# Performance work log

Hardware: AMD Instinct MI355X
Metric: run time of the kernel (lower is better)

The kernel has to match this reference:

```python
import jax, jax.numpy as jnp
import numpy as np

NEG_SLOPE = 0.2
EPS = 1e-16  # PyG softmax denominator epsilon


def add_self_loops(edge_index, num_nodes):
    loop = jnp.arange(num_nodes, dtype=edge_index.dtype)
    src = jnp.concatenate([edge_index[0], loop])
    dst = jnp.concatenate([edge_index[1], loop])
    return src, dst


def gat_conv(x, src, dst, W, att_src, att_dst, bias, num_nodes):
    H, C = att_src.shape
    h = (x @ W).reshape(num_nodes, H, C)            # [N,H,C]
    a_s = jnp.einsum('nhc,hc->nh', h, att_src)      # [N,H]
    a_d = jnp.einsum('nhc,hc->nh', h, att_dst)
    e = jax.nn.leaky_relu(a_s[src] + a_d[dst], NEG_SLOPE)  # [E,H]
    m = jax.ops.segment_max(e, dst, num_segments=num_nodes)
    e = jnp.exp(e - m[dst])
    s = jax.ops.segment_sum(e, dst, num_segments=num_nodes)
    alpha = e / (s[dst] + EPS)                      # [E,H]
    out = jax.ops.segment_sum(h[src] * alpha[:, :, None], dst,
                              num_segments=num_nodes)  # [N,H,C]
    return out.reshape(num_nodes, H * C) + bias


def setup_inputs() -> dict:
    key = jax.random.key(0)
    ks = jax.random.split(key, 10)
    N, E, F, Ch = 50000, 800000, 128, 64
    sc = lambda f: 1.0 / np.sqrt(f)
    return {
        'x': jax.random.normal(ks[0], (N, F), jnp.float32),
        'edge_index': jax.random.randint(ks[1], (2, E), 0, N, jnp.int64),
        'W1': jax.random.normal(ks[2], (F, 4 * Ch), jnp.float32) * sc(F),
        'att_src1': jax.random.normal(ks[3], (4, Ch), jnp.float32) * sc(Ch),
        'att_dst1': jax.random.normal(ks[4], (4, Ch), jnp.float32) * sc(Ch),
        'b1': jnp.zeros((4 * Ch,), jnp.float32),
        'W2': jax.random.normal(ks[5], (4 * Ch, Ch), jnp.float32) * sc(4 * Ch),
        'att_src2': jax.random.normal(ks[6], (1, Ch), jnp.float32) * sc(Ch),
        'att_dst2': jax.random.normal(ks[7], (1, Ch), jnp.float32) * sc(Ch),
        'b2': jnp.zeros((Ch,), jnp.float32),
    }


def reference(x, edge_index, W1, att_src1, att_dst1, b1, W2, att_src2, att_dst2, b2):
    N = x.shape[0]
    src, dst = add_self_loops(edge_index, N)
    # dropout layers are inference no-ops
    h = gat_conv(x, src, dst, W1, att_src1, att_dst1, b1, N)
    h = jax.nn.elu(h)
    out = gat_conv(h, src, dst, W2, att_src2, att_dst2, b2, N)
    return out
```

## Files before the change

kernel.cpp:

```cpp
#include <hip/hip_runtime.h>
#include <hip/hip_bf16.h>
#include <stdint.h>


typedef __attribute__((ext_vector_type(8))) short bf16x8;
typedef __attribute__((ext_vector_type(4))) float f32x4;

__device__ __forceinline__ float bf2f(__hip_bfloat16 v) { return __bfloat162float(v); }
__device__ __forceinline__ float bfbits2f(unsigned short s) {
  union { uint32_t u; float f; } v; v.u = ((uint32_t)s) << 16; return v.f;
}
__device__ __forceinline__ unsigned short f2bfbits(float f) {
  union { float f; uint32_t u; } v; v.f = f;
  uint32_t u = v.u;
  return (unsigned short)((u + 0x7fffu + ((u >> 16) & 1u)) >> 16);
}

template <bool BF>
__device__ __forceinline__ float loadF(const void* p, size_t i) {
  if (BF) return bf2f(((const __hip_bfloat16*)p)[i]);
  return ((const float*)p)[i];
}
template <bool BF>
__device__ __forceinline__ void storeF(void* p, size_t i, float v) {
  if (BF) ((__hip_bfloat16*)p)[i] = __float2bfloat16(v);
  else    ((float*)p)[i] = v;
}
template <bool I64>
__device__ __forceinline__ int loadI(const void* p, size_t i) {
  if (I64) return (int)((const long long*)p)[i];
  return ((const int*)p)[i];
}
__device__ __forceinline__ float lrelu(float v) { return fmaxf(v, 0.2f * v); }

__global__ void detect_kernel(const uint32_t* __restrict__ xbits,
                              const uint32_t* __restrict__ eibits,
                              int* __restrict__ flags) {
  if (threadIdx.x != 0 || blockIdx.x != 0) return;
  int plausible = 0;
  for (int i = 0; i < 64; i++) {
    uint32_t u = xbits[i];
    uint32_t e = (u >> 23) & 0xffu;
    if ((e < 160u && e > 90u) || (u & 0x7fffffffu) == 0u) plausible++;
  }
  flags[0] = (plausible < 32) ? 1 : 0;
  int allz = 1;
  for (int i = 0; i < 64; i++)
    if (eibits[2 * i + 1] != 0u) allz = 0;
  flags[1] = allz;
}

__global__ __launch_bounds__(256) void prep_all(
    const void* __restrict__ x, unsigned short* __restrict__ xb, size_t nx,
    const void* __restrict__ W1, unsigned short* __restrict__ w1t, int K1, int N1,
    const void* __restrict__ W2, unsigned short* __restrict__ w2t, int K2, int N2,
    int nb_cast, int nb_t1, const int* __restrict__ flags) {
  const int b = blockIdx.x;
  const bool f = flags[0] != 0;
  if (b < nb_cast) {
    size_t i = ((size_t)b * 256 + threadIdx.x) * 4;
    if (i >= nx) return;
    ushort4 o;
    if (f) {
      o = *(const ushort4*)((const unsigned short*)x + i);
    } else {
      float4 v = *(const float4*)((const float*)x + i);
      o.x = f2bfbits(v.x); o.y = f2bfbits(v.y);
      o.z = f2bfbits(v.z); o.w = f2bfbits(v.w);
    }
    *(ushort4*)(xb + i) = o;
  } else if (b < nb_cast + nb_t1) {
    int idx = (b - nb_cast) * 256 + threadIdx.x;
    if (idx >= K1 * N1) return;
    int k = idx / N1, n = idx - k * N1;
    float v = f ? loadF<true>(W1, idx) : loadF<false>(W1, idx);
    w1t[(size_t)n * K1 + k] = f2bfbits(v);
  } else {
    int idx = (b - nb_cast - nb_t1) * 256 + threadIdx.x;
    if (idx >= K2 * N2) return;
    int k = idx / N2, n = idx - k * N2;
    float v = f ? loadF<true>(W2, idx) : loadF<false>(W2, idx);
    w2t[(size_t)n * K2 + k] = f2bfbits(v);
  }
}

template <int KC, int NT, int HB>
__global__ __launch_bounds__(256, 4) void gemm_mfma_att(
    const unsigned short* __restrict__ A,
    const unsigned short* __restrict__ BT,
    unsigned short* __restrict__ C,
    const void* __restrict__ att_s, const void* __restrict__ att_d,
    float* __restrict__ as_o, float* __restrict__ ad_o,
    float* __restrict__ wself_o,
    int M, int Htot, const int* __restrict__ flags) {
  const int lane = threadIdx.x & 63;
  const int col = lane & 15;
  const int quad = lane >> 4;
  const int m0 = blockIdx.x * 64 + (threadIdx.x >> 6) * 16;
  const int n0 = blockIdx.y * (NT * 16);
  const int NCOL = Htot * 64;

  int gm = m0 + col;
  if (gm > M - 1) gm = M - 1;
  const unsigned short* arow = A + (size_t)gm * KC + quad * 8;
  const unsigned short* bbase = BT + (size_t)(n0 + col) * KC + quad * 8;

  f32x4 acc[NT] = {};
#pragma unroll
  for (int k0 = 0; k0 < KC; k0 += 32) {
    bf16x8 a = *(const bf16x8*)(arow + k0);
#pragma unroll
    for (int s = 0; s < NT; s++) {
      bf16x8 b = *(const bf16x8*)(bbase + (size_t)s * 16 * KC + k0);
      acc[s] = __builtin_amdgcn_mfma_f32_16x16x32_bf16(a, b, acc[s], 0, 0, 0);
    }
  }
#pragma unroll
  for (int s = 0; s < NT; s++)
#pragma unroll
    for (int r = 0; r < 4; r++) {
      int m = m0 + quad * 4 + r;
      if (m < M) C[(size_t)m * NCOL + n0 + s * 16 + col] = f2bfbits(acc[s][r]);
    }
  const int SC = NT / HB;
  const bool f = flags[0] != 0;
#pragma unroll
  for (int h = 0; h < HB; h++) {
    const int gh = blockIdx.y * HB + h;
    float ps[4] = {0.f, 0.f, 0.f, 0.f};
    float pd[4] = {0.f, 0.f, 0.f, 0.f};
#pragma unroll
    for (int j = 0; j < SC; j++) {
      int s = h * SC + j;
      int ci = gh * 64 + j * 16 + col;
      float av = f ? loadF<true>(att_s, ci) : loadF<false>(att_s, ci);
      float dv = f ? loadF<true>(att_d, ci) : loadF<false>(att_d, ci);
#pragma unroll
      for (int r = 0; r < 4; r++) {
        ps[r] += acc[s][r] * av;
        pd[r] += acc[s][r] * dv;
      }
    }
#pragma unroll
    for (int o = 1; o < 16; o <<= 1) {
#pragma unroll
      for (int r = 0; r < 4; r++) {
        ps[r] += __shfl_xor(ps[r], o);
        pd[r] += __shfl_xor(pd[r], o);
      }
    }
    if (col == 0) {
#pragma unroll
      for (int r = 0; r < 4; r++) {
        int m = m0 + quad * 4 + r;
        if (m < M) {
          as_o[m * Htot + gh] = ps[r];
          ad_o[m * Htot + gh] = pd[r];
          wself_o[m * Htot + gh] = __expf(lrelu(ps[r] + pd[r]));
        }
      }
    }
  }
}

__global__ void hist_kernel(const void* __restrict__ ei, int E,
                            int* __restrict__ deg, const int* __restrict__ flags) {
  int e = blockIdx.x * blockDim.x + threadIdx.x;
  if (e >= E) return;
  int d = flags[1] ? loadI<true>(ei, (size_t)E + e) : loadI<false>(ei, (size_t)E + e);
  atomicAdd(&deg[d], 1);
}

__global__ __launch_bounds__(256) void scan_block_sums(const int* __restrict__ deg,
                                                       int* __restrict__ bsum, int n) {
  __shared__ int buf[256];
  const int t = threadIdx.x;
  const int i = blockIdx.x * 256 + t;
  buf[t] = (i < n) ? deg[i] : 0;
  __syncthreads();
  for (int o = 128; o > 0; o >>= 1) {
    if (t < o) buf[t] += buf[t + o];
    __syncthreads();
  }
  if (t == 0) bsum[blockIdx.x] = buf[0];
}

__global__ __launch_bounds__(256) void scan_bsums(int* __restrict__ bsum, int nb) {
  __shared__ int buf[256];
  const int t = threadIdx.x;
  int orig = (t < nb) ? bsum[t] : 0;
  buf[t] = orig;
  __syncthreads();
  for (int o = 1; o < 256; o <<= 1) {
    int v = (t >= o) ? buf[t - o] : 0;
    __syncthreads();
    buf[t] += v;
    __syncthreads();
  }
  if (t < nb) bsum[t] = buf[t] - orig;
}

__global__ __launch_bounds__(256) void scan_finalize(const int* __restrict__ deg,
                                                     const int* __restrict__ bsum,
                                                     int* __restrict__ row_start, int n) {
  __shared__ int buf[256];
  const int t = threadIdx.x;
  const int i = blockIdx.x * 256 + t;
  int v = (i < n) ? deg[i] : 0;
  buf[t] = v;
  __syncthreads();
  for (int o = 1; o < 256; o <<= 1) {
    int x = (t >= o) ? buf[t - o] : 0;
    __syncthreads();
    buf[t] += x;
    __syncthreads();
  }
  if (i < n) row_start[i + 1] = bsum[blockIdx.x] + buf[t];
  if (i == 0) row_start[0] = 0;
}

__global__ void scatter_edges(const void* __restrict__ ei, int E,
                              const int* __restrict__ row_start,
                              int* __restrict__ cursor, int* __restrict__ col_src,
                              int* __restrict__ col_dst,
                              const int* __restrict__ flags) {
  int e = blockIdx.x * blockDim.x + threadIdx.x;
  if (e >= E) return;
  int s, d;
  if (flags[1]) { s = loadI<true>(ei, e);  d = loadI<true>(ei, (size_t)E + e); }
  else          { s = loadI<false>(ei, e); d = loadI<false>(ei, (size_t)E + e); }
  int pos = atomicAdd(&cursor[d], 1);
  int idx = row_start[d] + pos;
  col_src[idx] = s;
  col_dst[idx] = d;
}

__global__ __launch_bounds__(256) void weight4(
    const int* __restrict__ col_src, const int* __restrict__ col_dst,
    const float4* __restrict__ as4, const float4* __restrict__ ad4,
    float4* __restrict__ wbuf, int E) {
  int e = blockIdx.x * 256 + threadIdx.x;
  if (e >= E) return;
  float4 a = as4[col_src[e]];
  float4 b = ad4[col_dst[e]];
  float4 w;
  w.x = __expf(lrelu(a.x + b.x));
  w.y = __expf(lrelu(a.y + b.y));
  w.z = __expf(lrelu(a.z + b.z));
  w.w = __expf(lrelu(a.w + b.w));
  wbuf[e] = w;
}

__global__ __launch_bounds__(256) void weight1(
    const int* __restrict__ col_src, const int* __restrict__ col_dst,
    const float* __restrict__ as_, const float* __restrict__ ad_,
    float* __restrict__ wbuf, int E) {
  int e = blockIdx.x * 256 + threadIdx.x;
  if (e >= E) return;
  wbuf[e] = __expf(lrelu(as_[col_src[e]] + ad_[col_dst[e]]));
}

__global__ __launch_bounds__(256) void aggregate4(
    const unsigned short* __restrict__ h_in,
    const float* __restrict__ wselfA,
    const float* __restrict__ wbuf,
    const int* __restrict__ row_start, const int* __restrict__ col_src,
    const void* __restrict__ bias,
    unsigned short* __restrict__ out,
    int N, const int* __restrict__ flags) {
  const int dst = blockIdx.x * 4 + (threadIdx.x >> 6);
  if (dst >= N) return;
  const int l = threadIdx.x & 63;
  const int h = l >> 4;
  const int rs = row_start[dst];
  const int dg = row_start[dst + 1] - rs;
  const float ws = wselfA[dst * 4 + h];

  float a0, a1, a2, a3;
  {
    ushort4 sv = *(const ushort4*)(h_in + (size_t)dst * 256 + 4 * l);
    a0 = ws * bfbits2f(sv.x);
    a1 = ws * bfbits2f(sv.y);
    a2 = ws * bfbits2f(sv.z);
    a3 = ws * bfbits2f(sv.w);
  }
  float p = 0.f;
#pragma unroll 4
  for (int i = 0; i < dg; i++) {
    int sn = col_src[rs + i];
    float w = wbuf[(size_t)(rs + i) * 4 + h];
    p += w;
    ushort4 sv = *(const ushort4*)(h_in + (size_t)sn * 256 + 4 * l);
    a0 += w * bfbits2f(sv.x);
    a1 += w * bfbits2f(sv.y);
    a2 += w * bfbits2f(sv.z);
    a3 += w * bfbits2f(sv.w);
  }
  const float inv = 1.0f / (p + ws + 1e-16f);
  const bool f = flags[0] != 0;
  float b0, b1, b2, b3;
  if (f) {
    b0 = loadF<true>(bias, 4 * l + 0); b1 = loadF<true>(bias, 4 * l + 1);
    b2 = loadF<true>(bias, 4 * l + 2); b3 = loadF<true>(bias, 4 * l + 3);
  } else {
    b0 = loadF<false>(bias, 4 * l + 0); b1 = loadF<false>(bias, 4 * l + 1);
    b2 = loadF<false>(bias, 4 * l + 2); b3 = loadF<false>(bias, 4 * l + 3);
  }
  float o0 = a0 * inv + b0, o1 = a1 * inv + b1;
  float o2 = a2 * inv + b2, o3 = a3 * inv + b3;
  o0 = o0 > 0.f ? o0 : __expf(o0) - 1.f;
  o1 = o1 > 0.f ? o1 : __expf(o1) - 1.f;
  o2 = o2 > 0.f ? o2 : __expf(o2) - 1.f;
  o3 = o3 > 0.f ? o3 : __expf(o3) - 1.f;
  ushort4 ov;
  ov.x = f2bfbits(o0); ov.y = f2bfbits(o1); ov.z = f2bfbits(o2); ov.w = f2bfbits(o3);
  *(ushort4*)(out + (size_t)dst * 256 + 4 * l) = ov;
}

__global__ __launch_bounds__(256) void aggregate1(
    const unsigned short* __restrict__ h_in,
    const float* __restrict__ wselfA,
    const float* __restrict__ wbuf,
    const int* __restrict__ row_start, const int* __restrict__ col_src,
    const void* __restrict__ bias,
    void* __restrict__ out, int N, const int* __restrict__ flags) {
  const int dst = blockIdx.x * 4 + (threadIdx.x >> 6);
  if (dst >= N) return;
  const int l = threadIdx.x & 63;
  const int el = l & 15;
  const int slot = l >> 4;
  const int rs = row_start[dst];
  const int dg = row_start[dst + 1] - rs;
  const float ws = wselfA[dst];

  float a0 = 0.f, a1 = 0.f, a2 = 0.f, a3 = 0.f, p = 0.f;
  if (slot == 0) {
    ushort4 sv = *(const ushort4*)(h_in + (size_t)dst * 64 + 4 * el);
    a0 = ws * bfbits2f(sv.x);
    a1 = ws * bfbits2f(sv.y);
    a2 = ws * bfbits2f(sv.z);
    a3 = ws * bfbits2f(sv.w);
  }
#pragma unroll 2
  for (int i = slot; i < dg; i += 4) {
    int sn = col_src[rs + i];
    float w = wbuf[rs + i];
    p += w;
    ushort4 sv = *(const ushort4*)(h_in + (size_t)sn * 64 + 4 * el);
    a0 += w * bfbits2f(sv.x);
    a1 += w * bfbits2f(sv.y);
    a2 += w * bfbits2f(sv.z);
    a3 += w * bfbits2f(sv.w);
  }
  a0 += __shfl_xor(a0, 16); a0 += __shfl_xor(a0, 32);
  a1 += __shfl_xor(a1, 16); a1 += __shfl_xor(a1, 32);
  a2 += __shfl_xor(a2, 16); a2 += __shfl_xor(a2, 32);
  a3 += __shfl_xor(a3, 16); a3 += __shfl_xor(a3, 32);
  p  += __shfl_xor(p, 16);  p  += __shfl_xor(p, 32);

  if (slot == 0) {
    const float inv = 1.0f / (p + ws + 1e-16f);
    const bool f = flags[0] != 0;
    float b0, b1, b2, b3;
    if (f) {
      b0 = loadF<true>(bias, 4 * el + 0); b1 = loadF<true>(bias, 4 * el + 1);
      b2 = loadF<true>(bias, 4 * el + 2); b3 = loadF<true>(bias, 4 * el + 3);
    } else {
      b0 = loadF<false>(bias, 4 * el + 0); b1 = loadF<false>(bias, 4 * el + 1);
      b2 = loadF<false>(bias, 4 * el + 2); b3 = loadF<false>(bias, 4 * el + 3);
    }
    float o0 = a0 * inv + b0, o1 = a1 * inv + b1;
    float o2 = a2 * inv + b2, o3 = a3 * inv + b3;
    size_t ob = (size_t)dst * 64 + 4 * el;
    if (f) {
      ushort4 ov;
      ov.x = f2bfbits(o0); ov.y = f2bfbits(o1);
      ov.z = f2bfbits(o2); ov.w = f2bfbits(o3);
      *(ushort4*)((unsigned short*)out + ob) = ov;
    } else {
      float4 ov; ov.x = o0; ov.y = o1; ov.z = o2; ov.w = o3;
      *(float4*)((float*)out + ob) = ov;
    }
  }
}

extern "C" void kernel_launch(void* const* d_in, const int* in_sizes, int n_in,
                              void* d_out, int out_size, void* d_ws, size_t ws_size,
                              hipStream_t stream) {
  const void* x    = d_in[0];
  const void* ei   = d_in[1];
  const void* W1   = d_in[2];
  const void* as1w = d_in[3];
  const void* ad1w = d_in[4];
  const void* b1   = d_in[5];
  const void* W2   = d_in[6];
  const void* as2w = d_in[7];
  const void* ad2w = d_in[8];
  const void* b2   = d_in[9];

  const int N  = out_size / 64;
  const int F  = in_sizes[0] / N;
  const int E  = in_sizes[1] / 2;
  const int H1 = in_sizes[3] / 64;
  const int D1 = H1 * 64;
  const int D2 = 64;

  size_t off = 0;
  auto alloc = [&](size_t bytes) -> void* {
    void* p = (char*)d_ws + off;
    off += (bytes + 255) & ~(size_t)255;
    return p;
  };
  int* flags = (int*)alloc(2 * sizeof(int));
  __hip_bfloat16* h1 = (__hip_bfloat16*)alloc((size_t)N * D1 * 2);
  __hip_bfloat16* x2 = (__hip_bfloat16*)alloc((size_t)N * D1 * 2);
  __hip_bfloat16* h2 = h1;
  unsigned short* xb  = (unsigned short*)alloc((size_t)N * F * 2);
  unsigned short* w1t = (unsigned short*)alloc((size_t)D1 * F * 2);
  unsigned short* w2t = (unsigned short*)alloc((size_t)D2 * D1 * 2);
  float* as1 = (float*)alloc((size_t)N * H1 * 4);
  float* ad1 = (float*)alloc((size_t)N * H1 * 4);
  float* wself1 = (float*)alloc((size_t)N * H1 * 4);
  float* as2 = (float*)alloc((size_t)N * 4);
  float* ad2 = (float*)alloc((size_t)N * 4);
  float* wself2 = (float*)alloc((size_t)N * 4);
  int* zero_region = (int*)alloc((size_t)2 * N * 4);
  int* deg = zero_region;
  int* cursor = zero_region + N;
  int* row_start = (int*)alloc((size_t)(N + 1) * 4);
  int* col_src = (int*)alloc((size_t)E * 4);
  int* col_dst = (int*)alloc((size_t)E * 4);
  float* wbuf = (float*)alloc((size_t)E * 4 * 4);
  int* bsum = (int*)alloc((size_t)256 * 4);
  (void)ws_size; (void)n_in;

  const int nb = (N + 255) / 256;
  const int eb = (E + 255) / 256;
  const int db = (N + 3) / 4;
  const int gb = (N + 63) / 64;

  detect_kernel<<<1, 64, 0, stream>>>((const uint32_t*)x, (const uint32_t*)ei, flags);
  hipMemsetAsync(zero_region, 0, (size_t)2 * N * 4, stream);
  hist_kernel<<<eb, 256, 0, stream>>>(ei, E, deg, flags);
  scan_block_sums<<<nb, 256, 0, stream>>>(deg, bsum, N);
  scan_bsums<<<1, 256, 0, stream>>>(bsum, nb);
  scan_finalize<<<nb, 256, 0, stream>>>(deg, bsum, row_start, N);
  scatter_edges<<<eb, 256, 0, stream>>>(ei, E, row_start, cursor, col_src, col_dst, flags);

  const size_t nx = (size_t)N * F;
  const int nb_cast = (int)((nx / 4 + 255) / 256);
  const int nb_t1 = (F * D1 + 255) / 256;
  const int nb_t2 = (D1 * D2 + 255) / 256;
  prep_all<<<nb_cast + nb_t1 + nb_t2, 256, 0, stream>>>(
      x, xb, nx, W1, w1t, F, D1, W2, w2t, D1, D2, nb_cast, nb_t1, flags);

  gemm_mfma_att<128, 8, 2><<<dim3(gb, 2), 256, 0, stream>>>(
      xb, w1t, (unsigned short*)h1, as1w, ad1w, as1, ad1, wself1, N, H1, flags);
  weight4<<<eb, 256, 0, stream>>>(col_src, col_dst, (const float4*)as1,
                                  (const float4*)ad1, (float4*)wbuf, E);
  aggregate4<<<db, 256, 0, stream>>>((const unsigned short*)h1, wself1, wbuf,
                                     row_start, col_src, b1,
                                     (unsigned short*)x2, N, flags);

  gemm_mfma_att<256, 4, 1><<<dim3(gb, 1), 256, 0, stream>>>(
      (const unsigned short*)x2, w2t, (unsigned short*)h2, as2w, ad2w,
      as2, ad2, wself2, N, 1, flags);
  weight1<<<eb, 256, 0, stream>>>(col_src, col_dst, as2, ad2, wbuf, E);
  aggregate1<<<db, 256, 0, stream>>>((const unsigned short*)h2, wself2, wbuf,
                                     row_start, col_src, b2, d_out, N, flags);
}
```

Measured before the change: 349.4 us.

## Fuse edge attention weight computation into aggregation kernels and merge detect with zeroing

Removes the separate weight4/weight1 kernels and the per-edge wbuf and col_dst buffers. Each aggregation kernel now recomputes exp(leaky_relu(a_s[src]+a_d[dst])) inline from the gathered source index, so an E×4 float buffer no longer has to be written and read back. The format-detection kernel is parallelised with ballots and also zeroes the degree/cursor region, replacing a memset launch. In exchange the aggregate loops do extra scattered loads of a_s per edge and redundant exp work across the lanes of each head.

```diff
diff --git a/kernel.cpp b/kernel.cpp
--- a/kernel.cpp
+++ b/kernel.cpp
@@ -21,11 +21,6 @@
   if (BF) return bf2f(((const __hip_bfloat16*)p)[i]);
   return ((const float*)p)[i];
 }
-template <bool BF>
-__device__ __forceinline__ void storeF(void* p, size_t i, float v) {
-  if (BF) ((__hip_bfloat16*)p)[i] = __float2bfloat16(v);
-  else    ((float*)p)[i] = v;
-}
 template <bool I64>
 __device__ __forceinline__ int loadI(const void* p, size_t i) {
   if (I64) return (int)((const long long*)p)[i];
@@ -33,21 +28,27 @@
 }
 __device__ __forceinline__ float lrelu(float v) { return fmaxf(v, 0.2f * v); }
 
-__global__ void detect_kernel(const uint32_t* __restrict__ xbits,
-                              const uint32_t* __restrict__ eibits,
-                              int* __restrict__ flags) {
-  if (threadIdx.x != 0 || blockIdx.x != 0) return;
-  int plausible = 0;
-  for (int i = 0; i < 64; i++) {
-    uint32_t u = xbits[i];
-    uint32_t e = (u >> 23) & 0xffu;
-    if ((e < 160u && e > 90u) || (u & 0x7fffffffu) == 0u) plausible++;
-  }
-  flags[0] = (plausible < 32) ? 1 : 0;
-  int allz = 1;
-  for (int i = 0; i < 64; i++)
-    if (eibits[2 * i + 1] != 0u) allz = 0;
-  flags[1] = allz;
+__global__ __launch_bounds__(256) void detect_zero(
+    const uint32_t* __restrict__ xbits, const uint32_t* __restrict__ eibits,
+    int* __restrict__ flags, int* __restrict__ zero_region, int nzero) {
+  if (blockIdx.x == 0) {
+    if (threadIdx.x < 64) {
+      const int l = threadIdx.x;
+      uint32_t u = xbits[l];
+      uint32_t e = (u >> 23) & 0xffu;
+      bool plausible = (e < 160u && e > 90u) || (u & 0x7fffffffu) == 0u;
+      unsigned long long m1 = __ballot(plausible);
+      bool z = (eibits[2 * l + 1] == 0u);
+      unsigned long long m2 = __ballot(z);
+      if (l == 0) {
+        flags[0] = (__popcll(m1) < 32) ? 1 : 0;
+        flags[1] = (m2 == ~0ULL) ? 1 : 0;
+      }
+    }
+    return;
+  }
+  int i = (blockIdx.x - 1) * 256 + threadIdx.x;
+  if (i < nzero) zero_region[i] = 0;
 }
 
 __global__ __launch_bounds__(256) void prep_all(
@@ -222,7 +223,6 @@
 __global__ void scatter_edges(const void* __restrict__ ei, int E,
                               const int* __restrict__ row_start,
                               int* __restrict__ cursor, int* __restrict__ col_src,
-                              int* __restrict__ col_dst,
                               const int* __restrict__ flags) {
   int e = blockIdx.x * blockDim.x + threadIdx.x;
   if (e >= E) return;
@@ -230,40 +230,14 @@
   if (flags[1]) { s = loadI<true>(ei, e);  d = loadI<true>(ei, (size_t)E + e); }
   else          { s = loadI<false>(ei, e); d = loadI<false>(ei, (size_t)E + e); }
   int pos = atomicAdd(&cursor[d], 1);
-  int idx = row_start[d] + pos;
-  col_src[idx] = s;
-  col_dst[idx] = d;
-}
-
-__global__ __launch_bounds__(256) void weight4(
-    const int* __restrict__ col_src, const int* __restrict__ col_dst,
-    const float4* __restrict__ as4, const float4* __restrict__ ad4,
-    float4* __restrict__ wbuf, int E) {
-  int e = blockIdx.x * 256 + threadIdx.x;
-  if (e >= E) return;
-  float4 a = as4[col_src[e]];
-  float4 b = ad4[col_dst[e]];
-  float4 w;
-  w.x = __expf(lrelu(a.x + b.x));
-  w.y = __expf(lrelu(a.y + b.y));
-  w.z = __expf(lrelu(a.z + b.z));
-  w.w = __expf(lrelu(a.w + b.w));
-  wbuf[e] = w;
-}
-
-__global__ __launch_bounds__(256) void weight1(
-    const int* __restrict__ col_src, const int* __restrict__ col_dst,
-    const float* __restrict__ as_, const float* __restrict__ ad_,
-    float* __restrict__ wbuf, int E) {
-  int e = blockIdx.x * 256 + threadIdx.x;
-  if (e >= E) return;
-  wbuf[e] = __expf(lrelu(as_[col_src[e]] + ad_[col_dst[e]]));
+  col_src[row_start[d] + pos] = s;
 }
 
 __global__ __launch_bounds__(256) void aggregate4(
     const unsigned short* __restrict__ h_in,
     const float* __restrict__ wselfA,
-    const float* __restrict__ wbuf,
+    const float* __restrict__ as_,
+    const float* __restrict__ ad_,
     const int* __restrict__ row_start, const int* __restrict__ col_src,
     const void* __restrict__ bias,
     unsigned short* __restrict__ out,
@@ -275,6 +249,7 @@
   const int rs = row_start[dst];
   const int dg = row_start[dst + 1] - rs;
   const float ws = wselfA[dst * 4 + h];
+  const float adv = ad_[dst * 4 + h];
 
   float a0, a1, a2, a3;
   {
@@ -288,7 +263,7 @@
 #pragma unroll 4
   for (int i = 0; i < dg; i++) {
     int sn = col_src[rs + i];
-    float w = wbuf[(size_t)(rs + i) * 4 + h];
+    float w = __expf(lrelu(as_[(size_t)sn * 4 + h] + adv));
     p += w;
     ushort4 sv = *(const ushort4*)(h_in + (size_t)sn * 256 + 4 * l);
     a0 += w * bfbits2f(sv.x);
@@ -320,7 +295,8 @@
 __global__ __launch_bounds__(256) void aggregate1(
     const unsigned short* __restrict__ h_in,
     const float* __restrict__ wselfA,
-    const float* __restrict__ wbuf,
+    const float* __restrict__ as_,
+    const float* __restrict__ ad_,
     const int* __restrict__ row_start, const int* __restrict__ col_src,
     const void* __restrict__ bias,
     void* __restrict__ out, int N, const int* __restrict__ flags) {
@@ -332,6 +308,7 @@
   const int rs = row_start[dst];
   const int dg = row_start[dst + 1] - rs;
   const float ws = wselfA[dst];
+  const float adv = ad_[dst];
 
   float a0 = 0.f, a1 = 0.f, a2 = 0.f, a3 = 0.f, p = 0.f;
   if (slot == 0) {
@@ -344,7 +321,7 @@
 #pragma unroll 2
   for (int i = slot; i < dg; i += 4) {
     int sn = col_src[rs + i];
-    float w = wbuf[rs + i];
+    float w = __expf(lrelu(as_[sn] + adv));
     p += w;
     ushort4 sv = *(const ushort4*)(h_in + (size_t)sn * 64 + 4 * el);
     a0 += w * bfbits2f(sv.x);
@@ -429,8 +406,6 @@
   int* cursor = zero_region + N;
   int* row_start = (int*)alloc((size_t)(N + 1) * 4);
   int* col_src = (int*)alloc((size_t)E * 4);
-  int* col_dst = (int*)alloc((size_t)E * 4);
-  float* wbuf = (float*)alloc((size_t)E * 4 * 4);
   int* bsum = (int*)alloc((size_t)256 * 4);
   (void)ws_size; (void)n_in;
 
@@ -438,14 +413,16 @@
   const int eb = (E + 255) / 256;
   const int db = (N + 3) / 4;
   const int gb = (N + 63) / 64;
-
-  detect_kernel<<<1, 64, 0, stream>>>((const uint32_t*)x, (const uint32_t*)ei, flags);
-  hipMemsetAsync(zero_region, 0, (size_t)2 * N * 4, stream);
+  const int nzero = 2 * N;
+  const int zb = (nzero + 255) / 256;
+
+  detect_zero<<<1 + zb, 256, 0, stream>>>((const uint32_t*)x, (const uint32_t*)ei,
+                                          flags, zero_region, nzero);
   hist_kernel<<<eb, 256, 0, stream>>>(ei, E, deg, flags);
   scan_block_sums<<<nb, 256, 0, stream>>>(deg, bsum, N);
   scan_bsums<<<1, 256, 0, stream>>>(bsum, nb);
   scan_finalize<<<nb, 256, 0, stream>>>(deg, bsum, row_start, N);
-  scatter_edges<<<eb, 256, 0, stream>>>(ei, E, row_start, cursor, col_src, col_dst, flags);
+  scatter_edges<<<eb, 256, 0, stream>>>(ei, E, row_start, cursor, col_src, flags);
 
   const size_t nx = (size_t)N * F;
   const int nb_cast = (int)((nx / 4 + 255) / 256);
@@ -456,16 +433,13 @@
 
   gemm_mfma_att<128, 8, 2><<<dim3(gb, 2), 256, 0, stream>>>(
       xb, w1t, (unsigned short*)h1, as1w, ad1w, as1, ad1, wself1, N, H1, flags);
-  weight4<<<eb, 256, 0, stream>>>(col_src, col_dst, (const float4*)as1,
-                                  (const float4*)ad1, (float4*)wbuf, E);
-  aggregate4<<<db, 256, 0, stream>>>((const unsigned short*)h1, wself1, wbuf,
+  aggregate4<<<db, 256, 0, stream>>>((const unsigned short*)h1, wself1, as1, ad1,
                                      row_start, col_src, b1,
                                      (unsigned short*)x2, N, flags);
 
   gemm_mfma_att<256, 4, 1><<<dim3(gb, 1), 256, 0, stream>>>(
       (const unsigned short*)x2, w2t, (unsigned short*)h2, as2w, ad2w,
       as2, ad2, wself2, N, 1, flags);
-  weight1<<<eb, 256, 0, stream>>>(col_src, col_dst, as2, ad2, wbuf, E);
-  aggregate1<<<db, 256, 0, stream>>>((const unsigned short*)h2, wself2, wbuf,
+  aggregate1<<<db, 256, 0, stream>>>((const unsigned short*)h2, wself2, as2, ad2,
                                      row_start, col_src, b2, d_out, N, flags);
 }
```

Result: faster. 331.3 us (-5.2%).
